# Optimization experiments

Measured on AMD Instinct MI355X. Metric: run time of the kernel, lower is better.

## Reference

```python
import jax, jax.numpy as jnp
import numpy as np

B, N = 256, 16384


def setup_inputs() -> dict:
    key = jax.random.key(0)
    k1, k2, k3 = jax.random.split(key, 3)
    pred_coords = jax.random.normal(k1, (B, N, 3), dtype=jnp.float32)
    true_coords = jax.random.normal(k2, (B, N, 3), dtype=jnp.float32)
    weights = jax.random.uniform(k3, (B, N), dtype=jnp.float32)
    mask = jnp.ones((B, N), dtype=bool)
    return {"pred_coords": pred_coords, "true_coords": true_coords,
            "weights": weights, "mask": mask}


def reference(pred_coords, true_coords, weights, mask):
    # Mask out invalid atoms (Algorithm 28, weighted Kabsch alignment)
    pred = jnp.where(mask[..., None], pred_coords, 0.0)
    true = jnp.where(mask[..., None], true_coords, 0.0)
    w = jnp.where(mask, weights, 0.0)[..., None]            # [b, n, 1]

    wsum = w.sum(axis=1, keepdims=True)                     # [b, 1, 1]
    pred_centroid = (pred * w).sum(axis=1, keepdims=True) / wsum
    true_centroid = (true * w).sum(axis=1, keepdims=True) / wsum

    pred_c = pred - pred_centroid                           # [b, n, 3]
    true_c = true - true_centroid                           # [b, n, 3]

    # weighted covariance: [b, 3, 3]
    cov = jnp.einsum('bni,bnj->bij', true_c * w, pred_c)

    # torch.svd returns V (not V^T); jnp returns Vh = V^T. rot = U @ V^T = U @ Vh
    U, _, Vh = jnp.linalg.svd(cov)
    rot = jnp.einsum('bij,bjk->bik', U, Vh)

    # reflection fix: flip last column of V (= last row of Vh) where det < 0
    det = jnp.linalg.det(rot)                               # [b]
    flip = jnp.where(det < 0, -1.0, 1.0)                    # [b]
    Vh_fixed = Vh.at[:, -1, :].multiply(flip[:, None])
    rot = jnp.einsum('bij,bjk->bik', U, Vh_fixed)

    aligned = jnp.einsum('bni,bij->bnj', pred_c, rot) + true_centroid
    # original module calls .detach_() on the output
    return jax.lax.stop_gradient(aligned)
```

## Files before the change

### kernel.cpp

```cpp
#include <hip/hip_runtime.h>
#include <stdint.h>
#include <math.h>

constexpr int BATCH = 256;
constexpr int NATOM = 16384;
constexpr int TPB   = 256;
constexpr int NQ    = 16;
constexpr int C1    = 4;
constexpr int ABLK  = NATOM / C1;
constexpr int GRAN  = 4;

typedef float f32x4 __attribute__((ext_vector_type(4)));
typedef int   i32x4 __attribute__((ext_vector_type(4)));

__global__ __launch_bounds__(TPB) void wra_partials(
    const float* __restrict__ pred, const float* __restrict__ tru,
    const float* __restrict__ wgt, const int* __restrict__ mask,
    float* __restrict__ partials)
{
    const int blk = blockIdx.x;
    const int b   = blk >> 2;
    const int s   = blk & 3;
    const int tid = threadIdx.x;

    float acc[NQ];
    #pragma unroll
    for (int k = 0; k < NQ; ++k) acc[k] = 0.f;

    #pragma unroll 2
    for (int it = 0; it < GRAN; ++it) {
        const long base = (long)b * NATOM + (long)s * ABLK
                        + (long)it * (TPB * 4) + (long)tid * 4;

        const f32x4* p4 = reinterpret_cast<const f32x4*>(pred + base * 3);
        const f32x4* t4 = reinterpret_cast<const f32x4*>(tru  + base * 3);
        f32x4 pA = p4[0], pB = p4[1], pC = p4[2];
        f32x4 tA = t4[0], tB = t4[1], tC = t4[2];
        f32x4 wv = *reinterpret_cast<const f32x4*>(wgt + base);
        i32x4 mv = *reinterpret_cast<const i32x4*>(mask + base);

        const float pf[12] = {pA.x,pA.y,pA.z,pA.w, pB.x,pB.y,pB.z,pB.w,
                              pC.x,pC.y,pC.z,pC.w};
        const float tf[12] = {tA.x,tA.y,tA.z,tA.w, tB.x,tB.y,tB.z,tB.w,
                              tC.x,tC.y,tC.z,tC.w};
        const float wf[4]  = {wv.x, wv.y, wv.z, wv.w};
        const int   mf[4]  = {mv.x, mv.y, mv.z, mv.w};

        #pragma unroll
        for (int k = 0; k < 4; ++k) {
            const float w  = (mf[k] != 0) ? wf[k] : 0.f;
            const float px = pf[3*k], py = pf[3*k+1], pz = pf[3*k+2];
            const float tx = tf[3*k], ty = tf[3*k+1], tz = tf[3*k+2];
            const float wtx = w * tx, wty = w * ty, wtz = w * tz;
            acc[0]  += w;
            acc[1]  += w * px;  acc[2]  += w * py;  acc[3]  += w * pz;
            acc[4]  += wtx;     acc[5]  += wty;     acc[6]  += wtz;
            acc[7]  += wtx*px;  acc[8]  += wtx*py;  acc[9]  += wtx*pz;
            acc[10] += wty*px;  acc[11] += wty*py;  acc[12] += wty*pz;
            acc[13] += wtz*px;  acc[14] += wtz*py;  acc[15] += wtz*pz;
        }
    }

    #pragma unroll
    for (int off = 32; off >= 4; off >>= 1) {
        #pragma unroll
        for (int k = 0; k < NQ; ++k)
            acc[k] += __shfl_down(acc[k], off, 64);
    }
    __shared__ float red[16][NQ + 1];
    const int wave = tid >> 6, lane = tid & 63;
    if (lane < 4) {
        #pragma unroll
        for (int k = 0; k < NQ; ++k) red[wave * 4 + lane][k] = acc[k];
    }
    __syncthreads();
    if (tid < NQ) {
        float ssum = 0.f;
        #pragma unroll
        for (int r = 0; r < 16; ++r) ssum += red[r][tid];
        partials[blk * NQ + tid] = ssum;
    }
}

__device__ inline void jrot(double M[3][3], double V[3][3], int p, int q) {
    double mpq = M[p][q];
    if (fabs(mpq) < 1e-300) return;
    double theta = (M[q][q] - M[p][p]) / (2.0 * mpq);
    double t = copysign(1.0, theta) / (fabs(theta) + sqrt(theta * theta + 1.0));
    double c = 1.0 / sqrt(t * t + 1.0);
    double s = t * c;
    int r = 3 - p - q;
    double mpp = M[p][p], mqq = M[q][q], mrp = M[r][p], mrq = M[r][q];
    M[p][p] = mpp - t * mpq;
    M[q][q] = mqq + t * mpq;
    M[p][q] = M[q][p] = 0.0;
    double nrp = c * mrp - s * mrq;
    double nrq = s * mrp + c * mrq;
    M[r][p] = M[p][r] = nrp;
    M[r][q] = M[q][r] = nrq;
    #pragma unroll
    for (int i = 0; i < 3; ++i) {
        double vip = V[i][p], viq = V[i][q];
        V[i][p] = c * vip - s * viq;
        V[i][q] = s * vip + c * viq;
    }
}

__global__ __launch_bounds__(TPB) void wra_solve_apply(
    const float* __restrict__ pred, const int* __restrict__ mask,
    const float* __restrict__ partials, float* __restrict__ out)
{
    const int blk = blockIdx.x;
    const int b   = blk >> 2;
    const int s   = blk & 3;
    const int tid = threadIdx.x;

    __shared__ double q[NQ];
    __shared__ float cst[12];

    if (tid < NQ) {
        double sum = 0.0;
        #pragma unroll
        for (int c = 0; c < C1; ++c)
            sum += (double)partials[(b * C1 + c) * NQ + tid];
        q[tid] = sum;
    }
    __syncthreads();

    if (tid == 0) {
        const double wsum = q[0];
        double pc[3], tc[3];
        for (int j = 0; j < 3; ++j) { pc[j] = q[1+j] / wsum; tc[j] = q[4+j] / wsum; }

        double Cv[3][3];
        for (int i = 0; i < 3; ++i)
            for (int j = 0; j < 3; ++j)
                Cv[i][j] = q[7 + 3*i + j] - wsum * tc[i] * pc[j];

        double M[3][3];
        for (int i = 0; i < 3; ++i)
            for (int j = 0; j < 3; ++j)
                M[i][j] = Cv[0][i]*Cv[0][j] + Cv[1][i]*Cv[1][j] + Cv[2][i]*Cv[2][j];
        double V[3][3] = {{1,0,0},{0,1,0},{0,0,1}};
        for (int sweep = 0; sweep < 12; ++sweep) {
            double off = M[0][1]*M[0][1] + M[0][2]*M[0][2] + M[1][2]*M[1][2];
            double diag = M[0][0] + M[1][1] + M[2][2];
            if (off <= 1e-28 * diag * diag) break;
            jrot(M, V, 0, 1);
            jrot(M, V, 0, 2);
            jrot(M, V, 1, 2);
        }
        double lam[3] = {M[0][0], M[1][1], M[2][2]};
        int i0 = 0, i1 = 1, i2 = 2, tmp;
        if (lam[i0] < lam[i1]) { tmp = i0; i0 = i1; i1 = tmp; }
        if (lam[i0] < lam[i2]) { tmp = i0; i0 = i2; i2 = tmp; }
        if (lam[i1] < lam[i2]) { tmp = i1; i1 = i2; i2 = tmp; }
        double v0[3] = {V[0][i0], V[1][i0], V[2][i0]};
        double v1[3] = {V[0][i1], V[1][i1], V[2][i1]};
        double v2[3] = {V[0][i2], V[1][i2], V[2][i2]};

        double u0[3], u1[3];
        for (int i = 0; i < 3; ++i) {
            u0[i] = Cv[i][0]*v0[0] + Cv[i][1]*v0[1] + Cv[i][2]*v0[2];
            u1[i] = Cv[i][0]*v1[0] + Cv[i][1]*v1[1] + Cv[i][2]*v1[2];
        }
        double n0 = sqrt(u0[0]*u0[0] + u0[1]*u0[1] + u0[2]*u0[2]);
        for (int i = 0; i < 3; ++i) u0[i] /= n0;
        double d01 = u1[0]*u0[0] + u1[1]*u0[1] + u1[2]*u0[2];
        for (int i = 0; i < 3; ++i) u1[i] -= d01 * u0[i];
        double n1 = sqrt(u1[0]*u1[0] + u1[1]*u1[1] + u1[2]*u1[2]);
        for (int i = 0; i < 3; ++i) u1[i] /= n1;

        double detV = v0[0]*(v1[1]*v2[2] - v1[2]*v2[1])
                    - v0[1]*(v1[0]*v2[2] - v1[2]*v2[0])
                    + v0[2]*(v1[0]*v2[1] - v1[1]*v2[0]);
        double sV = (detV >= 0.0) ? 1.0 : -1.0;
        double u2[3] = { sV * (u0[1]*u1[2] - u0[2]*u1[1]),
                         sV * (u0[2]*u1[0] - u0[0]*u1[2]),
                         sV * (u0[0]*u1[1] - u0[1]*u1[0]) };

        double R[3][3];
        for (int i = 0; i < 3; ++i)
            for (int j = 0; j < 3; ++j)
                R[i][j] = u0[i]*v0[j] + u1[i]*v1[j] + u2[i]*v2[j];
        for (int i = 0; i < 3; ++i)
            for (int j = 0; j < 3; ++j)
                cst[3*i + j] = (float)R[i][j];
        for (int j = 0; j < 3; ++j)
            cst[9 + j] = (float)(tc[j] - (pc[0]*R[0][j] + pc[1]*R[1][j]
                                                        + pc[2]*R[2][j]));
    }
    __syncthreads();

    const float dx = cst[9], dy = cst[10], dz = cst[11];

    #pragma unroll 2
    for (int g = 0; g < GRAN; ++g) {
        const long base = (long)b * NATOM + (long)s * ABLK
                        + (long)g * (TPB * 4) + (long)tid * 4;
        const f32x4* p4 = reinterpret_cast<const f32x4*>(pred + base * 3);
        f32x4 P0 = p4[0], P1 = p4[1], P2 = p4[2];
        i32x4 mv = *reinterpret_cast<const i32x4*>(mask + base);

        const float pf[12] = {P0.x,P0.y,P0.z,P0.w, P1.x,P1.y,P1.z,P1.w,
                              P2.x,P2.y,P2.z,P2.w};
        const int   mf[4]  = {mv.x, mv.y, mv.z, mv.w};
        float O[12];
        #pragma unroll
        for (int k = 0; k < 4; ++k) {
            const float px = mf[k] ? pf[3*k]   : 0.f;
            const float py = mf[k] ? pf[3*k+1] : 0.f;
            const float pz = mf[k] ? pf[3*k+2] : 0.f;
            O[3*k]     = px * cst[0] + py * cst[3] + pz * cst[6] + dx;
            O[3*k + 1] = px * cst[1] + py * cst[4] + pz * cst[7] + dy;
            O[3*k + 2] = px * cst[2] + py * cst[5] + pz * cst[8] + dz;
        }
        f32x4* o4 = reinterpret_cast<f32x4*>(out + base * 3);
        f32x4 o0 = {O[0], O[1], O[2],  O[3]};
        f32x4 o1 = {O[4], O[5], O[6],  O[7]};
        f32x4 o2 = {O[8], O[9], O[10], O[11]};
        __builtin_nontemporal_store(o0, o4 + 0);
        __builtin_nontemporal_store(o1, o4 + 1);
        __builtin_nontemporal_store(o2, o4 + 2);
    }
}

extern "C" void kernel_launch(void* const* d_in, const int* in_sizes, int n_in,
                              void* d_out, int out_size, void* d_ws, size_t ws_size,
                              hipStream_t stream) {
    const float* pred = (const float*)d_in[0];
    const float* tru  = (const float*)d_in[1];
    const float* wgt  = (const float*)d_in[2];
    const int*   mask = (const int*)d_in[3];
    float* out = (float*)d_out;

    float* partials = (float*)d_ws;

    hipLaunchKernelGGL(wra_partials, dim3(BATCH * C1), dim3(TPB), 0, stream,
                       pred, tru, wgt, mask, partials);
    hipLaunchKernelGGL(wra_solve_apply, dim3(BATCH * C1), dim3(TPB), 0, stream,
                       pred, mask, partials, out);
}
```

Before: 204.3 us.

## Split Kabsch solve into separate kernel and widen grids for partials and apply

Moves the per-batch 3x3 SVD solve out of the apply kernel into a small kernel with one thread per batch, writing rotation and translation constants to workspace. The apply kernel now only loads those constants, so its blocks no longer wait behind a serial double-precision solve that was repeated in every block. The partials kernel uses 8 blocks per batch with both loads issued up front, and apply uses 16 blocks per batch with one tile each. The cost is an extra kernel launch and dependency.

```diff
diff --git a/kernel.cpp b/kernel.cpp
--- a/kernel.cpp
+++ b/kernel.cpp
@@ -6,9 +6,12 @@
 constexpr int NATOM = 16384;
 constexpr int TPB   = 256;
 constexpr int NQ    = 16;
-constexpr int C1    = 4;
-constexpr int ABLK  = NATOM / C1;
-constexpr int GRAN  = 4;
+
+constexpr int C1    = 8;
+constexpr int ABLK1 = NATOM / C1;
+
+constexpr int C3    = 16;
+constexpr int ABLK3 = NATOM / C3;
 
 typedef float f32x4 __attribute__((ext_vector_type(4)));
 typedef int   i32x4 __attribute__((ext_vector_type(4)));
@@ -19,33 +22,58 @@
     float* __restrict__ partials)
 {
     const int blk = blockIdx.x;
-    const int b   = blk >> 2;
-    const int s   = blk & 3;
+    const int b   = blk >> 3;
+    const int s   = blk & 7;
     const int tid = threadIdx.x;
+    const long baseA = (long)b * NATOM + (long)s * ABLK1 + (long)tid * 4;
+    const long baseB = baseA + TPB * 4;
+
+    const f32x4* pa4 = reinterpret_cast<const f32x4*>(pred + baseA * 3);
+    const f32x4* ta4 = reinterpret_cast<const f32x4*>(tru  + baseA * 3);
+    const f32x4* pb4 = reinterpret_cast<const f32x4*>(pred + baseB * 3);
+    const f32x4* tb4 = reinterpret_cast<const f32x4*>(tru  + baseB * 3);
+
+    f32x4 pA0 = pa4[0], pA1 = pa4[1], pA2 = pa4[2];
+    f32x4 tA0 = ta4[0], tA1 = ta4[1], tA2 = ta4[2];
+    f32x4 wA  = *reinterpret_cast<const f32x4*>(wgt + baseA);
+    i32x4 mA  = *reinterpret_cast<const i32x4*>(mask + baseA);
+    f32x4 pB0 = pb4[0], pB1 = pb4[1], pB2 = pb4[2];
+    f32x4 tB0 = tb4[0], tB1 = tb4[1], tB2 = tb4[2];
+    f32x4 wB  = *reinterpret_cast<const f32x4*>(wgt + baseB);
+    i32x4 mB  = *reinterpret_cast<const i32x4*>(mask + baseB);
 
     float acc[NQ];
     #pragma unroll
     for (int k = 0; k < NQ; ++k) acc[k] = 0.f;
 
-    #pragma unroll 2
-    for (int it = 0; it < GRAN; ++it) {
-        const long base = (long)b * NATOM + (long)s * ABLK
-                        + (long)it * (TPB * 4) + (long)tid * 4;
-
-        const f32x4* p4 = reinterpret_cast<const f32x4*>(pred + base * 3);
-        const f32x4* t4 = reinterpret_cast<const f32x4*>(tru  + base * 3);
-        f32x4 pA = p4[0], pB = p4[1], pC = p4[2];
-        f32x4 tA = t4[0], tB = t4[1], tC = t4[2];
-        f32x4 wv = *reinterpret_cast<const f32x4*>(wgt + base);
-        i32x4 mv = *reinterpret_cast<const i32x4*>(mask + base);
-
-        const float pf[12] = {pA.x,pA.y,pA.z,pA.w, pB.x,pB.y,pB.z,pB.w,
-                              pC.x,pC.y,pC.z,pC.w};
-        const float tf[12] = {tA.x,tA.y,tA.z,tA.w, tB.x,tB.y,tB.z,tB.w,
-                              tC.x,tC.y,tC.z,tC.w};
-        const float wf[4]  = {wv.x, wv.y, wv.z, wv.w};
-        const int   mf[4]  = {mv.x, mv.y, mv.z, mv.w};
-
+    {
+        const float pf[12] = {pA0.x,pA0.y,pA0.z,pA0.w, pA1.x,pA1.y,pA1.z,pA1.w,
+                              pA2.x,pA2.y,pA2.z,pA2.w};
+        const float tf[12] = {tA0.x,tA0.y,tA0.z,tA0.w, tA1.x,tA1.y,tA1.z,tA1.w,
+                              tA2.x,tA2.y,tA2.z,tA2.w};
+        const float wf[4]  = {wA.x, wA.y, wA.z, wA.w};
+        const int   mf[4]  = {mA.x, mA.y, mA.z, mA.w};
+        #pragma unroll
+        for (int k = 0; k < 4; ++k) {
+            const float w  = (mf[k] != 0) ? wf[k] : 0.f;
+            const float px = pf[3*k], py = pf[3*k+1], pz = pf[3*k+2];
+            const float tx = tf[3*k], ty = tf[3*k+1], tz = tf[3*k+2];
+            const float wtx = w * tx, wty = w * ty, wtz = w * tz;
+            acc[0]  += w;
+            acc[1]  += w * px;  acc[2]  += w * py;  acc[3]  += w * pz;
+            acc[4]  += wtx;     acc[5]  += wty;     acc[6]  += wtz;
+            acc[7]  += wtx*px;  acc[8]  += wtx*py;  acc[9]  += wtx*pz;
+            acc[10] += wty*px;  acc[11] += wty*py;  acc[12] += wty*pz;
+            acc[13] += wtz*px;  acc[14] += wtz*py;  acc[15] += wtz*pz;
+        }
+    }
+    {
+        const float pf[12] = {pB0.x,pB0.y,pB0.z,pB0.w, pB1.x,pB1.y,pB1.z,pB1.w,
+                              pB2.x,pB2.y,pB2.z,pB2.w};
+        const float tf[12] = {tB0.x,tB0.y,tB0.z,tB0.w, tB1.x,tB1.y,tB1.z,tB1.w,
+                              tB2.x,tB2.y,tB2.z,tB2.w};
+        const float wf[4]  = {wB.x, wB.y, wB.z, wB.w};
+        const int   mf[4]  = {mB.x, mB.y, mB.z, mB.w};
         #pragma unroll
         for (int k = 0; k < 4; ++k) {
             const float w  = (mf[k] != 0) ? wf[k] : 0.f;
@@ -106,123 +134,127 @@
     }
 }
 
-__global__ __launch_bounds__(TPB) void wra_solve_apply(
+__global__ __launch_bounds__(64) void wra_solve(
+    const float* __restrict__ partials, float* __restrict__ consts)
+{
+    const int b = blockIdx.x * 64 + threadIdx.x;
+    if (b >= BATCH) return;
+
+    double q[NQ];
+    #pragma unroll
+    for (int k = 0; k < NQ; ++k) {
+        double sum = 0.0;
+        #pragma unroll
+        for (int c = 0; c < C1; ++c)
+            sum += (double)partials[(b * C1 + c) * NQ + k];
+        q[k] = sum;
+    }
+
+    const double wsum = q[0];
+    double pc[3], tc[3];
+    for (int j = 0; j < 3; ++j) { pc[j] = q[1+j] / wsum; tc[j] = q[4+j] / wsum; }
+
+    double Cv[3][3];
+    for (int i = 0; i < 3; ++i)
+        for (int j = 0; j < 3; ++j)
+            Cv[i][j] = q[7 + 3*i + j] - wsum * tc[i] * pc[j];
+
+    double M[3][3];
+    for (int i = 0; i < 3; ++i)
+        for (int j = 0; j < 3; ++j)
+            M[i][j] = Cv[0][i]*Cv[0][j] + Cv[1][i]*Cv[1][j] + Cv[2][i]*Cv[2][j];
+    double V[3][3] = {{1,0,0},{0,1,0},{0,0,1}};
+    for (int sweep = 0; sweep < 12; ++sweep) {
+        double off = M[0][1]*M[0][1] + M[0][2]*M[0][2] + M[1][2]*M[1][2];
+        double diag = M[0][0] + M[1][1] + M[2][2];
+        if (off <= 1e-28 * diag * diag) break;
+        jrot(M, V, 0, 1);
+        jrot(M, V, 0, 2);
+        jrot(M, V, 1, 2);
+    }
+    double lam[3] = {M[0][0], M[1][1], M[2][2]};
+    int i0 = 0, i1 = 1, i2 = 2, tmp;
+    if (lam[i0] < lam[i1]) { tmp = i0; i0 = i1; i1 = tmp; }
+    if (lam[i0] < lam[i2]) { tmp = i0; i0 = i2; i2 = tmp; }
+    if (lam[i1] < lam[i2]) { tmp = i1; i1 = i2; i2 = tmp; }
+    double v0[3] = {V[0][i0], V[1][i0], V[2][i0]};
+    double v1[3] = {V[0][i1], V[1][i1], V[2][i1]};
+    double v2[3] = {V[0][i2], V[1][i2], V[2][i2]};
+
+    double u0[3], u1[3];
+    for (int i = 0; i < 3; ++i) {
+        u0[i] = Cv[i][0]*v0[0] + Cv[i][1]*v0[1] + Cv[i][2]*v0[2];
+        u1[i] = Cv[i][0]*v1[0] + Cv[i][1]*v1[1] + Cv[i][2]*v1[2];
+    }
+    double n0 = sqrt(u0[0]*u0[0] + u0[1]*u0[1] + u0[2]*u0[2]);
+    for (int i = 0; i < 3; ++i) u0[i] /= n0;
+    double d01 = u1[0]*u0[0] + u1[1]*u0[1] + u1[2]*u0[2];
+    for (int i = 0; i < 3; ++i) u1[i] -= d01 * u0[i];
+    double n1 = sqrt(u1[0]*u1[0] + u1[1]*u1[1] + u1[2]*u1[2]);
+    for (int i = 0; i < 3; ++i) u1[i] /= n1;
+
+    double detV = v0[0]*(v1[1]*v2[2] - v1[2]*v2[1])
+                - v0[1]*(v1[0]*v2[2] - v1[2]*v2[0])
+                + v0[2]*(v1[0]*v2[1] - v1[1]*v2[0]);
+    double sV = (detV >= 0.0) ? 1.0 : -1.0;
+    double u2[3] = { sV * (u0[1]*u1[2] - u0[2]*u1[1]),
+                     sV * (u0[2]*u1[0] - u0[0]*u1[2]),
+                     sV * (u0[0]*u1[1] - u0[1]*u1[0]) };
+
+    double R[3][3];
+    for (int i = 0; i < 3; ++i)
+        for (int j = 0; j < 3; ++j)
+            R[i][j] = u0[i]*v0[j] + u1[i]*v1[j] + u2[i]*v2[j];
+
+    float* o = consts + b * 12;
+    for (int i = 0; i < 3; ++i)
+        for (int j = 0; j < 3; ++j)
+            o[3*i + j] = (float)R[i][j];
+    for (int j = 0; j < 3; ++j)
+        o[9 + j] = (float)(tc[j] - (pc[0]*R[0][j] + pc[1]*R[1][j]
+                                                  + pc[2]*R[2][j]));
+}
+
+__global__ __launch_bounds__(TPB) void wra_apply(
     const float* __restrict__ pred, const int* __restrict__ mask,
-    const float* __restrict__ partials, float* __restrict__ out)
+    const float* __restrict__ consts, float* __restrict__ out)
 {
     const int blk = blockIdx.x;
-    const int b   = blk >> 2;
-    const int s   = blk & 3;
+    const int b   = blk >> 4;
+    const int s   = blk & 15;
     const int tid = threadIdx.x;
 
-    __shared__ double q[NQ];
     __shared__ float cst[12];
-
-    if (tid < NQ) {
-        double sum = 0.0;
-        #pragma unroll
-        for (int c = 0; c < C1; ++c)
-            sum += (double)partials[(b * C1 + c) * NQ + tid];
-        q[tid] = sum;
-    }
+    if (tid < 12) cst[tid] = consts[b * 12 + tid];
     __syncthreads();
 
-    if (tid == 0) {
-        const double wsum = q[0];
-        double pc[3], tc[3];
-        for (int j = 0; j < 3; ++j) { pc[j] = q[1+j] / wsum; tc[j] = q[4+j] / wsum; }
-
-        double Cv[3][3];
-        for (int i = 0; i < 3; ++i)
-            for (int j = 0; j < 3; ++j)
-                Cv[i][j] = q[7 + 3*i + j] - wsum * tc[i] * pc[j];
-
-        double M[3][3];
-        for (int i = 0; i < 3; ++i)
-            for (int j = 0; j < 3; ++j)
-                M[i][j] = Cv[0][i]*Cv[0][j] + Cv[1][i]*Cv[1][j] + Cv[2][i]*Cv[2][j];
-        double V[3][3] = {{1,0,0},{0,1,0},{0,0,1}};
-        for (int sweep = 0; sweep < 12; ++sweep) {
-            double off = M[0][1]*M[0][1] + M[0][2]*M[0][2] + M[1][2]*M[1][2];
-            double diag = M[0][0] + M[1][1] + M[2][2];
-            if (off <= 1e-28 * diag * diag) break;
-            jrot(M, V, 0, 1);
-            jrot(M, V, 0, 2);
-            jrot(M, V, 1, 2);
-        }
-        double lam[3] = {M[0][0], M[1][1], M[2][2]};
-        int i0 = 0, i1 = 1, i2 = 2, tmp;
-        if (lam[i0] < lam[i1]) { tmp = i0; i0 = i1; i1 = tmp; }
-        if (lam[i0] < lam[i2]) { tmp = i0; i0 = i2; i2 = tmp; }
-        if (lam[i1] < lam[i2]) { tmp = i1; i1 = i2; i2 = tmp; }
-        double v0[3] = {V[0][i0], V[1][i0], V[2][i0]};
-        double v1[3] = {V[0][i1], V[1][i1], V[2][i1]};
-        double v2[3] = {V[0][i2], V[1][i2], V[2][i2]};
-
-        double u0[3], u1[3];
-        for (int i = 0; i < 3; ++i) {
-            u0[i] = Cv[i][0]*v0[0] + Cv[i][1]*v0[1] + Cv[i][2]*v0[2];
-            u1[i] = Cv[i][0]*v1[0] + Cv[i][1]*v1[1] + Cv[i][2]*v1[2];
-        }
-        double n0 = sqrt(u0[0]*u0[0] + u0[1]*u0[1] + u0[2]*u0[2]);
-        for (int i = 0; i < 3; ++i) u0[i] /= n0;
-        double d01 = u1[0]*u0[0] + u1[1]*u0[1] + u1[2]*u0[2];
-        for (int i = 0; i < 3; ++i) u1[i] -= d01 * u0[i];
-        double n1 = sqrt(u1[0]*u1[0] + u1[1]*u1[1] + u1[2]*u1[2]);
-        for (int i = 0; i < 3; ++i) u1[i] /= n1;
-
-        double detV = v0[0]*(v1[1]*v2[2] - v1[2]*v2[1])
-                    - v0[1]*(v1[0]*v2[2] - v1[2]*v2[0])
-                    + v0[2]*(v1[0]*v2[1] - v1[1]*v2[0]);
-        double sV = (detV >= 0.0) ? 1.0 : -1.0;
-        double u2[3] = { sV * (u0[1]*u1[2] - u0[2]*u1[1]),
-                         sV * (u0[2]*u1[0] - u0[0]*u1[2]),
-                         sV * (u0[0]*u1[1] - u0[1]*u1[0]) };
-
-        double R[3][3];
-        for (int i = 0; i < 3; ++i)
-            for (int j = 0; j < 3; ++j)
-                R[i][j] = u0[i]*v0[j] + u1[i]*v1[j] + u2[i]*v2[j];
-        for (int i = 0; i < 3; ++i)
-            for (int j = 0; j < 3; ++j)
-                cst[3*i + j] = (float)R[i][j];
-        for (int j = 0; j < 3; ++j)
-            cst[9 + j] = (float)(tc[j] - (pc[0]*R[0][j] + pc[1]*R[1][j]
-                                                        + pc[2]*R[2][j]));
-    }
-    __syncthreads();
-
+    const long base = (long)b * NATOM + (long)s * ABLK3 + (long)tid * 4;
+    const f32x4* p4 = reinterpret_cast<const f32x4*>(pred + base * 3);
+    f32x4 P0 = p4[0], P1 = p4[1], P2 = p4[2];
+    i32x4 mv = *reinterpret_cast<const i32x4*>(mask + base);
+
+    const float pf[12] = {P0.x,P0.y,P0.z,P0.w, P1.x,P1.y,P1.z,P1.w,
+                          P2.x,P2.y,P2.z,P2.w};
+    const int   mf[4]  = {mv.x, mv.y, mv.z, mv.w};
     const float dx = cst[9], dy = cst[10], dz = cst[11];
 
-    #pragma unroll 2
-    for (int g = 0; g < GRAN; ++g) {
-        const long base = (long)b * NATOM + (long)s * ABLK
-                        + (long)g * (TPB * 4) + (long)tid * 4;
-        const f32x4* p4 = reinterpret_cast<const f32x4*>(pred + base * 3);
-        f32x4 P0 = p4[0], P1 = p4[1], P2 = p4[2];
-        i32x4 mv = *reinterpret_cast<const i32x4*>(mask + base);
-
-        const float pf[12] = {P0.x,P0.y,P0.z,P0.w, P1.x,P1.y,P1.z,P1.w,
-                              P2.x,P2.y,P2.z,P2.w};
-        const int   mf[4]  = {mv.x, mv.y, mv.z, mv.w};
-        float O[12];
-        #pragma unroll
-        for (int k = 0; k < 4; ++k) {
-            const float px = mf[k] ? pf[3*k]   : 0.f;
-            const float py = mf[k] ? pf[3*k+1] : 0.f;
-            const float pz = mf[k] ? pf[3*k+2] : 0.f;
-            O[3*k]     = px * cst[0] + py * cst[3] + pz * cst[6] + dx;
-            O[3*k + 1] = px * cst[1] + py * cst[4] + pz * cst[7] + dy;
-            O[3*k + 2] = px * cst[2] + py * cst[5] + pz * cst[8] + dz;
-        }
-        f32x4* o4 = reinterpret_cast<f32x4*>(out + base * 3);
-        f32x4 o0 = {O[0], O[1], O[2],  O[3]};
-        f32x4 o1 = {O[4], O[5], O[6],  O[7]};
-        f32x4 o2 = {O[8], O[9], O[10], O[11]};
-        __builtin_nontemporal_store(o0, o4 + 0);
-        __builtin_nontemporal_store(o1, o4 + 1);
-        __builtin_nontemporal_store(o2, o4 + 2);
-    }
+    float O[12];
+    #pragma unroll
+    for (int k = 0; k < 4; ++k) {
+        const float px = mf[k] ? pf[3*k]   : 0.f;
+        const float py = mf[k] ? pf[3*k+1] : 0.f;
+        const float pz = mf[k] ? pf[3*k+2] : 0.f;
+        O[3*k]     = px * cst[0] + py * cst[3] + pz * cst[6] + dx;
+        O[3*k + 1] = px * cst[1] + py * cst[4] + pz * cst[7] + dy;
+        O[3*k + 2] = px * cst[2] + py * cst[5] + pz * cst[8] + dz;
+    }
+    f32x4* o4 = reinterpret_cast<f32x4*>(out + base * 3);
+    f32x4 o0 = {O[0], O[1], O[2],  O[3]};
+    f32x4 o1 = {O[4], O[5], O[6],  O[7]};
+    f32x4 o2 = {O[8], O[9], O[10], O[11]};
+    __builtin_nontemporal_store(o0, o4 + 0);
+    __builtin_nontemporal_store(o1, o4 + 1);
+    __builtin_nontemporal_store(o2, o4 + 2);
 }
 
 extern "C" void kernel_launch(void* const* d_in, const int* in_sizes, int n_in,
@@ -235,9 +267,12 @@
     float* out = (float*)d_out;
 
     float* partials = (float*)d_ws;
+    float* consts   = partials + BATCH * C1 * NQ;
 
     hipLaunchKernelGGL(wra_partials, dim3(BATCH * C1), dim3(TPB), 0, stream,
                        pred, tru, wgt, mask, partials);
-    hipLaunchKernelGGL(wra_solve_apply, dim3(BATCH * C1), dim3(TPB), 0, stream,
-                       pred, mask, partials, out);
-}
+    hipLaunchKernelGGL(wra_solve, dim3(BATCH / 64), dim3(64), 0, stream,
+                       partials, consts);
+    hipLaunchKernelGGL(wra_apply, dim3(BATCH * C3), dim3(TPB), 0, stream,
+                       pred, mask, consts, out);
+}
```

Measured after the change: 190.5 us. 6.8% less time.
